# Optimization experiments

Measured on AMD Instinct MI355X. Metric: run time of the kernel, lower is better.

## Reference

```python
import jax, jax.numpy as jnp
import numpy as np

N = 100000
E = 1000000
IN_F, HID, NCLS = 128, 128, 40
EPS = 1e-5


def _gconv(h, src, dst, W, b):
    # DGL GraphConv with norm='both', allow_zero_in_degree=True (degrees clamped to >=1).
    ones = jnp.ones(src.shape, jnp.float32)
    dout = jnp.clip(jax.ops.segment_sum(ones, src, num_segments=N), 1.0)   # out-degree of src nodes
    din = jnp.clip(jax.ops.segment_sum(ones, dst, num_segments=N), 1.0)    # in-degree of dst nodes
    x = (h * jax.lax.rsqrt(dout)[:, None]) @ W            # [N, out] matmul-first (linear commutes with sum-aggregation)
    y = jax.ops.segment_sum(x[src], dst, num_segments=N)  # SpMM: scatter-add over edges
    y = y * jax.lax.rsqrt(din)[:, None]
    return y + b if b is not None else y


def _bn(h, gamma, beta):
    # BatchNorm1d training-mode math over the node dimension (biased variance).
    m = jnp.mean(h, axis=0)
    v = jnp.mean(jnp.square(h - m), axis=0)
    return (h - m) * jax.lax.rsqrt(v + EPS) * gamma + beta


def setup_inputs() -> dict:
    key = jax.random.key(0)
    ks = jax.random.split(key, 16)
    feat = jax.random.normal(ks[0], (N, IN_F), jnp.float32)
    src0 = jax.random.randint(ks[1], (E,), 0, N, jnp.int32)
    dst0 = jax.random.randint(ks[2], (E,), 0, N, jnp.int32)
    src1 = jax.random.randint(ks[3], (E,), 0, N, jnp.int32)
    dst1 = jax.random.randint(ks[4], (E,), 0, N, jnp.int32)
    order_attn = jax.random.uniform(ks[5], (2,), jnp.float32)
    s = lambda d_in, d_out: 1.0 / np.sqrt(d_in)
    W0 = jax.random.uniform(ks[6], (IN_F, HID), jnp.float32, -s(IN_F, HID), s(IN_F, HID))
    W1 = jax.random.uniform(ks[7], (HID, HID), jnp.float32, -s(HID, HID), s(HID, HID))
    W2 = jax.random.uniform(ks[8], (HID, NCLS), jnp.float32, -s(HID, NCLS), s(HID, NCLS))
    b2 = jnp.zeros((NCLS,), jnp.float32)
    L0 = jax.random.uniform(ks[9], (IN_F, HID), jnp.float32, -s(IN_F, HID), s(IN_F, HID))
    L1 = jax.random.uniform(ks[10], (HID, HID), jnp.float32, -s(HID, HID), s(HID, HID))
    L2 = jax.random.uniform(ks[11], (HID, NCLS), jnp.float32, -s(HID, NCLS), s(HID, NCLS))
    gamma0 = jnp.ones((HID,), jnp.float32); beta0 = jnp.zeros((HID,), jnp.float32)
    gamma1 = jnp.ones((HID,), jnp.float32); beta1 = jnp.zeros((HID,), jnp.float32)
    return dict(feat=feat, src0=src0, dst0=dst0, src1=src1, dst1=dst1, order_attn=order_attn,
                W0=W0, W1=W1, W2=W2, b2=b2, L0=L0, L1=L1, L2=L2,
                gamma0=gamma0, beta0=beta0, gamma1=gamma1, beta1=beta1)


def reference(feat, src0, dst0, src1, dst1, order_attn, W0, W1, W2, b2, L0, L1, L2,
              gamma0, beta0, gamma1, beta1):
    # Multi-graph path (len(graph)==2, n_layers==3, use_linear=True); dropout = identity (eval).
    h = feat
    # layer 0: order_attn-weighted combination of two adjacency variants
    conv1 = _gconv(h, src0, dst0, W0, None)
    conv2 = _gconv(h, src1, dst1, W0, None)
    conv = order_attn[0] * conv1 + order_attn[1] * conv2
    h = conv + h @ L0
    h = jax.nn.relu(_bn(h, gamma0, beta0))
    # layer 1 (convs[-2]) on graph[0]
    h = _gconv(h, src0, dst0, W1, None) + h @ L1
    h = jax.nn.relu(_bn(h, gamma1, beta1))
    # layer 2 (convs[-1]) on graph[0], with bias
    h = _gconv(h, src0, dst0, W2, b2) + h @ L2
    return h
```

## Files before the change

kernel.cpp:

```cpp
#include <hip/hip_runtime.h>
#include <math.h>

#define N_NODES 100000
#define N_EDGES 1000000
#define F 128
#define NC 40
#define BN_EPS 1e-5f
#define CH 32
#define EC (N_EDGES / CH)
#define WIN0 65536
#define NB1 (N_NODES - WIN0)
#define PROW (N_NODES / 4)

typedef unsigned int uint;
typedef unsigned short ushort;
typedef __attribute__((ext_vector_type(8))) short vbf8;
typedef __attribute__((ext_vector_type(4))) float vf4;

__device__ __forceinline__ float bf_lo(uint v) { return __uint_as_float(v << 16); }
__device__ __forceinline__ float bf_hi(uint v) { return __uint_as_float(v & 0xffff0000u); }
__device__ __forceinline__ ushort f2bf(float f) {
  uint u = __float_as_uint(f);
  u = u + 0x7fffu + ((u >> 16) & 1u);
  return (ushort)(u >> 16);
}
__device__ __forceinline__ uint pk2(float a, float b) {
  return (uint)f2bf(a) | ((uint)f2bf(b) << 16);
}

__global__ __launch_bounds__(256) void hist_count_k(
    const int* __restrict__ s0, const int* __restrict__ d0,
    const int* __restrict__ s1, const int* __restrict__ d1,
    unsigned* __restrict__ partial) {
  __shared__ unsigned bins[16384];
  int c = blockIdx.x, w = blockIdx.y, a = blockIdx.z;
  const int* keys = (a == 0) ? s0 : (a == 1) ? d0 : (a == 2) ? s1 : d1;
  int base = w * WIN0;
  int nb = w ? NB1 : WIN0;
  int nwords = nb >> 2;
  int t = threadIdx.x;
  for (int i = t; i < nwords; i += 256) bins[i] = 0;
  __syncthreads();
  int e0 = c * EC;
  for (int e = e0 + t; e < e0 + EC; e += 256) {
    int b = keys[e] - base;
    if ((unsigned)b < (unsigned)nb)
      atomicAdd(&bins[b >> 2], 1u << ((b & 3) * 8));
  }
  __syncthreads();
  unsigned* dst = partial + (size_t)(a * CH + c) * PROW + (w ? (WIN0 >> 2) : 0);
  for (int i = t; i < nwords; i += 256) dst[i] = bins[i];
}

__global__ __launch_bounds__(256) void deg_reduce_k(
    unsigned* __restrict__ partial, float* __restrict__ rs4, ushort* __restrict__ rsO01u,
    int* __restrict__ degIn0, int* __restrict__ degIn1,
    float* __restrict__ st0, float* __restrict__ st1) {
  int word = blockIdx.x * 256 + threadIdx.x;
  if (blockIdx.y == 0 && word < 256) { st0[word] = 0.f; st1[word] = 0.f; }
  if (word >= PROW) return;
  int a = blockIdx.y;
  bool din = (a == 1) || (a == 3);
  unsigned r0 = 0, r1 = 0, r2 = 0, r3 = 0;
  unsigned* rowp = partial + (size_t)a * CH * PROW + word;
  for (int c = 0; c < CH; ++c) {
    unsigned* p = rowp + (size_t)c * PROW;
    unsigned v = *p;
    if (din) *p = r0 | (r1 << 8) | (r2 << 16) | (r3 << 24);
    r0 += v & 255u; r1 += (v >> 8) & 255u; r2 += (v >> 16) & 255u; r3 += (v >> 24) & 255u;
  }
  int b = word * 4;
  float4 r;
  r.x = rsqrtf((float)max(r0, 1u));
  r.y = rsqrtf((float)max(r1, 1u));
  r.z = rsqrtf((float)max(r2, 1u));
  r.w = rsqrtf((float)max(r3, 1u));
  *(float4*)&rs4[(size_t)a * N_NODES + b] = r;
  if (a == 0) {
    rsO01u[2 * (b + 0)] = f2bf(r.x); rsO01u[2 * (b + 1)] = f2bf(r.y);
    rsO01u[2 * (b + 2)] = f2bf(r.z); rsO01u[2 * (b + 3)] = f2bf(r.w);
  }
  if (a == 2) {
    rsO01u[2 * (b + 0) + 1] = f2bf(r.x); rsO01u[2 * (b + 1) + 1] = f2bf(r.y);
    rsO01u[2 * (b + 2) + 1] = f2bf(r.z); rsO01u[2 * (b + 3) + 1] = f2bf(r.w);
  }
  if (a == 1) { degIn0[b] = r0; degIn0[b + 1] = r1; degIn0[b + 2] = r2; degIn0[b + 3] = r3; }
  if (a == 3) { degIn1[b] = r0; degIn1[b + 1] = r1; degIn1[b + 2] = r2; degIn1[b + 3] = r3; }
}

__global__ void scan_local_k(const int* __restrict__ cnt0, const int* __restrict__ cnt1,
                             int* __restrict__ out0, int* __restrict__ out1,
                             int* __restrict__ bsum) {
  __shared__ int lds[256];
  const int* cnt = blockIdx.y ? cnt1 : cnt0;
  int* out = blockIdx.y ? out1 : out0;
  int base = blockIdx.x * 2048;
  int t = threadIdx.x;
  int v[8];
  int s = 0;
#pragma unroll
  for (int j = 0; j < 8; ++j) {
    int idx = base + t * 8 + j;
    v[j] = (idx < N_NODES) ? cnt[idx] : 0;
    s += v[j];
  }
  lds[t] = s;
  __syncthreads();
  for (int off = 1; off < 256; off <<= 1) {
    int x = (t >= off) ? lds[t - off] : 0;
    __syncthreads();
    lds[t] += x;
    __syncthreads();
  }
  int excl = lds[t] - s;
  if (t == 255) bsum[blockIdx.y * 64 + blockIdx.x] = lds[255];
  int run = excl;
#pragma unroll
  for (int j = 0; j < 8; ++j) {
    int idx = base + t * 8 + j;
    if (idx < N_NODES) out[idx] = run;
    run += v[j];
  }
}

__global__ void scan_top_k(int* bsum, int nb) {
  int w = threadIdx.x >> 6, t = threadIdx.x & 63;
  int* b = bsum + w * 64;
  int orig = (t < nb) ? b[t] : 0;
  int v = orig;
  for (int off = 1; off < 64; off <<= 1) {
    int u = __shfl_up(v, off);
    if (t >= off) v += u;
  }
  if (t < nb) b[t] = v - orig;
}

__global__ void scan_apply_k(int* __restrict__ rp0, int* __restrict__ rp1,
                             const int* __restrict__ bsum) {
  int* rp = blockIdx.y ? rp1 : rp0;
  const int* bs = bsum + blockIdx.y * 64;
  int i = blockIdx.x * 256 + threadIdx.x;
  if (i < N_NODES) rp[i] += bs[i >> 11];
  if (i == 0) rp[N_NODES] = N_EDGES;
}

__global__ __launch_bounds__(256) void csr_fill2_k(
    const int* __restrict__ src0, const int* __restrict__ dst0, const int* __restrict__ rp0g,
    int* __restrict__ csr0g,
    const int* __restrict__ src1, const int* __restrict__ dst1, const int* __restrict__ rp1g,
    int* __restrict__ csr1g, const unsigned* __restrict__ partial) {
  __shared__ unsigned bins[16384];
  int c = blockIdx.x, w = blockIdx.y, g = blockIdx.z;
  const int* src = g ? src1 : src0;
  const int* dst = g ? dst1 : dst0;
  const int* rp = g ? rp1g : rp0g;
  int* csr = g ? csr1g : csr0g;
  int aIdx = g ? 3 : 1;
  int base = w * WIN0;
  int nb = w ? NB1 : WIN0;
  int nwords = nb >> 2;
  const unsigned* sp = partial + (size_t)(aIdx * CH + c) * PROW + (w ? (WIN0 >> 2) : 0);
  int t = threadIdx.x;
  for (int i = t; i < nwords; i += 256) bins[i] = sp[i];
  __syncthreads();
  int e0 = c * EC;
  for (int e = e0 + t; e < e0 + EC; e += 256) {
    int d = dst[e];
    int b = d - base;
    if ((unsigned)b < (unsigned)nb) {
      int sh = (b & 3) * 8;
      unsigned old = atomicAdd(&bins[b >> 2], 1u << sh);
      int off = (old >> sh) & 255;
      csr[rp[d] + off] = src[e];
    }
  }
}

__global__ __launch_bounds__(256) void pack_all_k(
    const float* __restrict__ x, uint* __restrict__ y,
    const float* __restrict__ Wa, const float* __restrict__ Wb,
    const float* __restrict__ Wc, const float* __restrict__ Wd,
    ushort* __restrict__ pk) {
  int b = blockIdx.x;
  int t = threadIdx.x;
  if (b < 1024) {
    size_t total = (size_t)N_NODES * F / 8;
    for (size_t idx = b * 256 + t; idx < total; idx += (size_t)1024 * 256) {
      float4 v1 = ((const float4*)x)[idx * 2];
      float4 v2 = ((const float4*)x)[idx * 2 + 1];
      uint4 o;
      o.x = pk2(v1.x, v1.y);
      o.y = pk2(v1.z, v1.w);
      o.z = pk2(v2.x, v2.y);
      o.w = pk2(v2.z, v2.w);
      ((uint4*)y)[idx] = o;
    }
  } else {
    int bb = b - 1024;
    int m = bb >> 3;
    int idx = (bb & 7) * 256 + t;
    const float* W = (m == 0) ? Wa : (m == 1) ? Wb : (m == 2) ? Wc : Wd;
    int lane = idx & 63;
    int nt = (idx >> 6) & 7;
    int ks = idx >> 9;
    int j = (lane & 15) + nt * 16;
    int kb = (lane >> 4) * 8 + ks * 32;
    ushort v[8];
#pragma unroll
    for (int q = 0; q < 8; ++q) v[q] = f2bf(W[(size_t)(kb + q) * F + j]);
    *(uint4*)(pk + (size_t)m * 16384 + (size_t)idx * 8) = *(uint4*)v;
  }
}

__global__ __launch_bounds__(256) void gather_dual_half_k(
    const uint* __restrict__ xbf, const float* __restrict__ attn,
    const uint* __restrict__ rsO01,
    const float* __restrict__ rsI0, const int* __restrict__ rp0, const int* __restrict__ csr0,
    const float* __restrict__ rsI1, const int* __restrict__ rp1, const int* __restrict__ csr1,
    uint* __restrict__ outbf) {
  int node = blockIdx.x * 4 + (threadIdx.x >> 6);
  int lane = threadIdx.x & 63;
  int half = lane >> 5, l = lane & 31;
  int b0 = rp0[node], n0 = rp0[node + 1] - b0;
  int b1 = rp1[node], n1 = rp1[node + 1] - b1;
  int T = n0 + n1;
  int h = (T + 1) >> 1;
  int e = half ? h : 0;
  int eend = half ? T : h;
  float w0 = attn[0] * rsI0[node];
  float w1 = attn[1] * rsI1[node];
  const int* p0 = csr0 + b0;
  const int* p1 = csr1 + b1 - n0;
  const uint2* xr = (const uint2*)xbf;
  float a0 = 0.f, a1 = 0.f, a2 = 0.f, a3 = 0.f;
  for (; e + 1 < eend; e += 2) {
    bool gA = e >= n0, gB = (e + 1) >= n0;
    int sA = (gA ? p1 : p0)[e];
    int sB = (gB ? p1 : p0)[e + 1];
    uint rA = rsO01[sA], rB = rsO01[sB];
    float cA = gA ? w1 * bf_hi(rA) : w0 * bf_lo(rA);
    float cB = gB ? w1 * bf_hi(rB) : w0 * bf_lo(rB);
    uint2 vA = xr[(size_t)sA * 32 + l];
    uint2 vB = xr[(size_t)sB * 32 + l];
    a0 = fmaf(bf_lo(vA.x), cA, a0); a1 = fmaf(bf_hi(vA.x), cA, a1);
    a2 = fmaf(bf_lo(vA.y), cA, a2); a3 = fmaf(bf_hi(vA.y), cA, a3);
    a0 = fmaf(bf_lo(vB.x), cB, a0); a1 = fmaf(bf_hi(vB.x), cB, a1);
    a2 = fmaf(bf_lo(vB.y), cB, a2); a3 = fmaf(bf_hi(vB.y), cB, a3);
  }
  if (e < eend) {
    bool gA = e >= n0;
    int sA = (gA ? p1 : p0)[e];
    uint rA = rsO01[sA];
    float cA = gA ? w1 * bf_hi(rA) : w0 * bf_lo(rA);
    uint2 vA = xr[(size_t)sA * 32 + l];
    a0 = fmaf(bf_lo(vA.x), cA, a0); a1 = fmaf(bf_hi(vA.x), cA, a1);
    a2 = fmaf(bf_lo(vA.y), cA, a2); a3 = fmaf(bf_hi(vA.y), cA, a3);
  }
  a0 += __shfl_xor(a0, 32);
  a1 += __shfl_xor(a1, 32);
  a2 += __shfl_xor(a2, 32);
  a3 += __shfl_xor(a3, 32);
  if (half == 0)
    ((uint2*)outbf)[(size_t)node * 32 + l] = make_uint2(pk2(a0, a1), pk2(a2, a3));
}

__global__ __launch_bounds__(256) void gather_half_k(
    const uint* __restrict__ xbf, const float* __restrict__ rsI,
    const int* __restrict__ rp, const int* __restrict__ csr,
    uint* __restrict__ outbf) {
  int node = blockIdx.x * 4 + (threadIdx.x >> 6);
  int lane = threadIdx.x & 63;
  int half = lane >> 5, l = lane & 31;
  int b0 = rp[node], T = rp[node + 1] - b0;
  int h = (T + 1) >> 1;
  int e = half ? h : 0;
  int eend = half ? T : h;
  const int* p = csr + b0;
  const uint2* xr = (const uint2*)xbf;
  float a0 = 0.f, a1 = 0.f, a2 = 0.f, a3 = 0.f;
  for (; e + 1 < eend; e += 2) {
    int sA = p[e], sB = p[e + 1];
    uint2 vA = xr[(size_t)sA * 32 + l];
    uint2 vB = xr[(size_t)sB * 32 + l];
    a0 += bf_lo(vA.x) + bf_lo(vB.x);
    a1 += bf_hi(vA.x) + bf_hi(vB.x);
    a2 += bf_lo(vA.y) + bf_lo(vB.y);
    a3 += bf_hi(vA.y) + bf_hi(vB.y);
  }
  if (e < eend) {
    int sA = p[e];
    uint2 vA = xr[(size_t)sA * 32 + l];
    a0 += bf_lo(vA.x); a1 += bf_hi(vA.x);
    a2 += bf_lo(vA.y); a3 += bf_hi(vA.y);
  }
  a0 += __shfl_xor(a0, 32);
  a1 += __shfl_xor(a1, 32);
  a2 += __shfl_xor(a2, 32);
  a3 += __shfl_xor(a3, 32);
  float sd = rsI[node];
  if (half == 0)
    ((uint2*)outbf)[(size_t)node * 32 + l] =
        make_uint2(pk2(a0 * sd, a1 * sd), pk2(a2 * sd, a3 * sd));
}

__global__ void gather40_add_k(const uint* __restrict__ x2bf, const float* __restrict__ rsI,
                               const int* __restrict__ rp, const int* __restrict__ csr,
                               float* __restrict__ out) {
  int node = (blockIdx.x * 256 + threadIdx.x) >> 5;
  int lane = threadIdx.x & 31;
  if (node >= N_NODES || lane >= 20) return;
  float l = 0.f, h = 0.f;
  int e = rp[node], end = rp[node + 1];
  for (; e + 3 < end; e += 4) {
    int sA = csr[e], sB = csr[e + 1], sC = csr[e + 2], sD = csr[e + 3];
    uint vA = x2bf[(size_t)sA * 20 + lane];
    uint vB = x2bf[(size_t)sB * 20 + lane];
    uint vC = x2bf[(size_t)sC * 20 + lane];
    uint vD = x2bf[(size_t)sD * 20 + lane];
    l += (bf_lo(vA) + bf_lo(vB)) + (bf_lo(vC) + bf_lo(vD));
    h += (bf_hi(vA) + bf_hi(vB)) + (bf_hi(vC) + bf_hi(vD));
  }
  for (; e < end; ++e) {
    uint vA = x2bf[(size_t)csr[e] * 20 + lane];
    l += bf_lo(vA);
    h += bf_hi(vA);
  }
  float sd = rsI[node];
  float2 p = *(float2*)(out + (size_t)node * NC + lane * 2);
  *(float2*)(out + (size_t)node * NC + lane * 2) = make_float2(p.x + l * sd, p.y + h * sd);
}

__global__ __launch_bounds__(256) void zscale_bf_k(
    const uint* __restrict__ h, const float* __restrict__ st,
    const float* __restrict__ gamma, const float* __restrict__ beta,
    const float* __restrict__ rs, uint* __restrict__ r0row, uint* __restrict__ zrow) {
  __shared__ float scl[128], shl[128];
  int t = threadIdx.x;
  if (t < 128) {
    float m = st[t] / (float)N_NODES;
    float v = st[128 + t] / (float)N_NODES - m * m;
    float s = gamma[t] * rsqrtf(fmaxf(v, 0.f) + BN_EPS);
    scl[t] = s;
    shl[t] = beta[t] - m * s;
  }
  __syncthreads();
  int idx = blockIdx.x * 256 + t;
  if (idx >= N_NODES * 16) return;
  int row = idx >> 4, kk = (idx & 15) * 8;
  uint4 v = ((const uint4*)h)[idx];
  float4 sc1 = *(float4*)&scl[kk];
  float4 sh1 = *(float4*)&shl[kk];
  float4 sc2 = *(float4*)&scl[kk + 4];
  float4 sh2 = *(float4*)&shl[kk + 4];
  float a0 = fmaxf(fmaf(bf_lo(v.x), sc1.x, sh1.x), 0.f);
  float a1 = fmaxf(fmaf(bf_hi(v.x), sc1.y, sh1.y), 0.f);
  float a2 = fmaxf(fmaf(bf_lo(v.y), sc1.z, sh1.z), 0.f);
  float a3 = fmaxf(fmaf(bf_hi(v.y), sc1.w, sh1.w), 0.f);
  float a4 = fmaxf(fmaf(bf_lo(v.z), sc2.x, sh2.x), 0.f);
  float a5 = fmaxf(fmaf(bf_hi(v.z), sc2.y, sh2.y), 0.f);
  float a6 = fmaxf(fmaf(bf_lo(v.w), sc2.z, sh2.z), 0.f);
  float a7 = fmaxf(fmaf(bf_hi(v.w), sc2.w, sh2.w), 0.f);
  uint4 o;
  o.x = pk2(a0, a1); o.y = pk2(a2, a3); o.z = pk2(a4, a5); o.w = pk2(a6, a7);
  ((uint4*)r0row)[idx] = o;
  float s = rs[row];
  uint4 z;
  z.x = pk2(a0 * s, a1 * s); z.y = pk2(a2 * s, a3 * s);
  z.z = pk2(a4 * s, a5 * s); z.w = pk2(a6 * s, a7 * s);
  ((uint4*)zrow)[idx] = z;
}

__global__ __launch_bounds__(256) void gemm_mfma_k(
    const ushort* __restrict__ A1, const ushort* __restrict__ A2,
    const ushort* __restrict__ pkA, const ushort* __restrict__ pkB,
    float* __restrict__ st, ushort* __restrict__ Cb) {
  __shared__ float sst[256];
  int t = threadIdx.x;
  int wave = t >> 6, lane = t & 63;
  int kgrp = lane >> 4, lrow = lane & 15;
  int arow = blockIdx.x * 64 + wave * 16 + lrow;
  bool rok = arow < N_NODES;
  const vbf8* a1p = (const vbf8*)(A1 + (size_t)(rok ? arow : 0) * F);
  const vbf8* a2p = (const vbf8*)(A2 + (size_t)(rok ? arow : 0) * F);
  const vbf8* wap = (const vbf8*)pkA + lane;
  const vbf8* wbp = (const vbf8*)pkB + lane;
  sst[t] = 0.f;
  __syncthreads();
  vbf8 zero = {0, 0, 0, 0, 0, 0, 0, 0};
  vf4 acc[8];
#pragma unroll
  for (int i = 0; i < 8; ++i) acc[i] = (vf4){0.f, 0.f, 0.f, 0.f};
#pragma unroll
  for (int ks = 0; ks < 4; ++ks) {
    vbf8 a1 = rok ? a1p[ks * 4 + kgrp] : zero;
    vbf8 a2 = rok ? a2p[ks * 4 + kgrp] : zero;
#pragma unroll
    for (int nt = 0; nt < 8; ++nt)
      acc[nt] = __builtin_amdgcn_mfma_f32_16x16x32_bf16(a1, wap[(ks * 8 + nt) * 64], acc[nt], 0, 0, 0);
#pragma unroll
    for (int nt = 0; nt < 8; ++nt)
      acc[nt] = __builtin_amdgcn_mfma_f32_16x16x32_bf16(a2, wbp[(ks * 8 + nt) * 64], acc[nt], 0, 0, 0);
  }
  int rbase = blockIdx.x * 64 + wave * 16 + kgrp * 4;
#pragma unroll
  for (int nt = 0; nt < 8; ++nt) {
    int col = nt * 16 + lrow;
#pragma unroll
    for (int r = 0; r < 4; ++r) {
      int row = rbase + r;
      if (row < N_NODES) Cb[(size_t)row * F + col] = f2bf(acc[nt][r]);
    }
  }
#pragma unroll
  for (int nt = 0; nt < 8; ++nt) {
    float s = acc[nt][0] + acc[nt][1] + acc[nt][2] + acc[nt][3];
    float q = acc[nt][0] * acc[nt][0] + acc[nt][1] * acc[nt][1] +
              acc[nt][2] * acc[nt][2] + acc[nt][3] * acc[nt][3];
    s += __shfl_xor(s, 16); q += __shfl_xor(q, 16);
    s += __shfl_xor(s, 32); q += __shfl_xor(q, 32);
    if (lane < 16) {
      atomicAdd(&sst[nt * 16 + lane], s);
      atomicAdd(&sst[128 + nt * 16 + lane], q);
    }
  }
  __syncthreads();
  atomicAdd(&st[t], sst[t]);
}

__global__ __launch_bounds__(256) void gemm40_dual_k(
    const uint* __restrict__ h1b, const float* __restrict__ st,
    const float* __restrict__ gamma, const float* __restrict__ beta,
    const float* __restrict__ W2, const float* __restrict__ L2, const float* __restrict__ bias,
    const float* __restrict__ rsO, uint* __restrict__ x2bf, float* __restrict__ outp) {
  __shared__ float Alds[25 * 128];
  __shared__ float Wl[128 * NC];
  __shared__ float Ll[128 * NC];
  __shared__ float scl[128], shl[128];
  int t = threadIdx.x;
  int r0 = blockIdx.x * 25;
  if (t < 128) {
    float m = st[t] / (float)N_NODES;
    float v = st[128 + t] / (float)N_NODES - m * m;
    float s = gamma[t] * rsqrtf(fmaxf(v, 0.f) + BN_EPS);
    scl[t] = s;
    shl[t] = beta[t] - m * s;
  }
  __syncthreads();
#pragma unroll
  for (int p = 0; p < 4; ++p) {
    int flat = t * 4 + p * 1024;
    if (flat < 25 * 128) {
      int lrr = flat >> 7, k = flat & 127;
      int row = r0 + lrr;
      float4 v = make_float4(0.f, 0.f, 0.f, 0.f);
      if (row < N_NODES) {
        uint2 u = *(const uint2*)(h1b + (size_t)row * 64 + (k >> 1));
        v = make_float4(bf_lo(u.x), bf_hi(u.x), bf_lo(u.y), bf_hi(u.y));
      }
      float4 scv = *(float4*)&scl[k];
      float4 shv = *(float4*)&shl[k];
      v.x = fmaxf(fmaf(v.x, scv.x, shv.x), 0.f);
      v.y = fmaxf(fmaf(v.y, scv.y, shv.y), 0.f);
      v.z = fmaxf(fmaf(v.z, scv.z, shv.z), 0.f);
      v.w = fmaxf(fmaf(v.w, scv.w, shv.w), 0.f);
      *(float4*)&Alds[flat] = v;
    }
  }
#pragma unroll
  for (int p = 0; p < 5; ++p) {
    int flat = t * 4 + p * 1024;
    if (flat < 128 * NC) {
      *(float4*)&Wl[flat] = *(const float4*)(W2 + flat);
      *(float4*)&Ll[flat] = *(const float4*)(L2 + flat);
    }
  }
  __syncthreads();
  if (t < 250) {
    int lrr = t / 10, cg = t % 10;
    float w0 = 0.f, w1 = 0.f, w2 = 0.f, w3 = 0.f;
    float l0 = 0.f, l1 = 0.f, l2 = 0.f, l3 = 0.f;
#pragma unroll 8
    for (int k = 0; k < 128; ++k) {
      float a = Alds[lrr * 128 + k];
      float4 w = *(float4*)&Wl[k * NC + cg * 4];
      float4 l = *(float4*)&Ll[k * NC + cg * 4];
      w0 = fmaf(a, w.x, w0); w1 = fmaf(a, w.y, w1);
      w2 = fmaf(a, w.z, w2); w3 = fmaf(a, w.w, w3);
      l0 = fmaf(a, l.x, l0); l1 = fmaf(a, l.y, l1);
      l2 = fmaf(a, l.z, l2); l3 = fmaf(a, l.w, l3);
    }
    int row = r0 + lrr;
    if (row < N_NODES) {
      float s = rsO[row];
      uint2 xo = make_uint2(pk2(w0 * s, w1 * s), pk2(w2 * s, w3 * s));
      *(uint2*)(x2bf + (size_t)row * 20 + cg * 2) = xo;
      float4 bv = *(const float4*)(bias + cg * 4);
      float4 oo = make_float4(l0 + bv.x, l1 + bv.y, l2 + bv.z, l3 + bv.w);
      *(float4*)(outp + (size_t)row * NC + cg * 4) = oo;
    }
  }
}

extern "C" void kernel_launch(void* const* d_in, const int* in_sizes, int n_in,
                              void* d_out, int out_size, void* d_ws, size_t ws_size,
                              hipStream_t stream) {
  const float* feat = (const float*)d_in[0];
  const int* src0 = (const int*)d_in[1];
  const int* dst0 = (const int*)d_in[2];
  const int* src1 = (const int*)d_in[3];
  const int* dst1 = (const int*)d_in[4];
  const float* attn = (const float*)d_in[5];
  const float* W0 = (const float*)d_in[6];
  const float* W1 = (const float*)d_in[7];
  const float* W2 = (const float*)d_in[8];
  const float* b2 = (const float*)d_in[9];
  const float* L0 = (const float*)d_in[10];
  const float* L1 = (const float*)d_in[11];
  const float* L2 = (const float*)d_in[12];
  const float* gamma0 = (const float*)d_in[13];
  const float* beta0 = (const float*)d_in[14];
  const float* gamma1 = (const float*)d_in[15];
  const float* beta1 = (const float*)d_in[16];
  float* out = (float*)d_out;

  char* base = (char*)d_ws;
  size_t off = 0;
  auto alloc = [&](size_t bytes) -> void* {
    void* p = base + off;
    off += (bytes + 255) & ~(size_t)255;
    return p;
  };
  unsigned* partial = (unsigned*)alloc((size_t)4 * CH * PROW * 4);
  float* rs4 = (float*)alloc(4 * (size_t)N_NODES * 4);
  uint* rsO01 = (uint*)alloc((size_t)N_NODES * 4);
  int* degIn0 = (int*)alloc(N_NODES * 4);
  int* degIn1 = (int*)alloc(N_NODES * 4);
  int* rp0 = (int*)alloc((N_NODES + 1) * 4);
  int* rp1 = (int*)alloc((N_NODES + 1) * 4);
  int* bsum = (int*)alloc(128 * 4);
  int* csr0 = (int*)alloc((size_t)N_EDGES * 4);
  int* csr1 = (int*)alloc((size_t)N_EDGES * 4);
  float* st0 = (float*)alloc(256 * 4);
  float* st1 = (float*)alloc(256 * 4);
  ushort* wpk = (ushort*)alloc((size_t)4 * 16384 * 2);
  uint* featbf = (uint*)alloc((size_t)N_NODES * 64 * 4);
  uint* aggbf = (uint*)alloc((size_t)N_NODES * 64 * 4);
  uint* hrow = (uint*)alloc((size_t)N_NODES * 64 * 4);
  uint* g1buf = (uint*)alloc((size_t)N_NODES * 64 * 4);
  if (off > ws_size) return;

  uint* r0row = aggbf;
  uint* zrow = featbf;
  uint* x2bf = featbf;

  float* rs_out0 = rs4;
  float* rs_in0 = rs4 + N_NODES;
  float* rs_in1 = rs4 + 3 * N_NODES;

  hist_count_k<<<dim3(CH, 2, 4), 256, 0, stream>>>(src0, dst0, src1, dst1, partial);
  deg_reduce_k<<<dim3((PROW + 255) / 256, 4), 256, 0, stream>>>(
      partial, rs4, (ushort*)rsO01, degIn0, degIn1, st0, st1);
  const int SCB = (N_NODES + 2047) / 2048;
  scan_local_k<<<dim3(SCB, 2), 256, 0, stream>>>(degIn0, degIn1, rp0, rp1, bsum);
  scan_top_k<<<1, 128, 0, stream>>>(bsum, SCB);
  scan_apply_k<<<dim3((N_NODES + 255) / 256, 2), 256, 0, stream>>>(rp0, rp1, bsum);
  csr_fill2_k<<<dim3(CH, 2, 2), 256, 0, stream>>>(src0, dst0, rp0, csr0,
                                                  src1, dst1, rp1, csr1, partial);

  pack_all_k<<<1056, 256, 0, stream>>>(feat, featbf, W0, L0, W1, L1, wpk);

  const int GB = (N_NODES + 63) / 64;

  gather_dual_half_k<<<N_NODES / 4, 256, 0, stream>>>(featbf, attn, rsO01, rs_in0, rp0, csr0,
                                                      rs_in1, rp1, csr1, aggbf);
  gemm_mfma_k<<<GB, 256, 0, stream>>>((ushort*)aggbf, (ushort*)featbf, wpk, wpk + 16384,
                                      st0, (ushort*)hrow);

  zscale_bf_k<<<N_NODES * 16 / 256, 256, 0, stream>>>(hrow, st0, gamma0, beta0, rs_out0,
                                                      r0row, zrow);
  gather_half_k<<<N_NODES / 4, 256, 0, stream>>>(zrow, rs_in0, rp0, csr0, g1buf);
  gemm_mfma_k<<<GB, 256, 0, stream>>>((ushort*)g1buf, (ushort*)r0row, wpk + 2 * 16384,
                                      wpk + 3 * 16384, st1, (ushort*)hrow);

  gemm40_dual_k<<<(N_NODES + 24) / 25, 256, 0, stream>>>(hrow, st1, gamma1, beta1, W2, L2, b2,
                                                         rs_out0, x2bf, out);
  gather40_add_k<<<(N_NODES * 32 + 255) / 256, 256, 0, stream>>>(x2bf, rs_in0, rp0, csr0, out);
}
```

Measured before the change: 520.5 us.

## Fuse BatchNorm+ReLU into layer-1 gather and GEMM, drop zscale pass

Removes the standalone zscale kernel that wrote normalized and degree-scaled bf16 copies of the hidden state. The layer-1 gather now applies BN scale/shift, ReLU and the source out-degree scale per gathered edge. A new GEMM variant applies BN+ReLU to its second operand while loading it. Gather loops in both gather kernels are also unrolled to four edges for more memory-level parallelism. This saves a full read and two full writes of the hidden matrix, in exchange for extra per-edge ALU work and an in-place hrow read/write in the GEMM that is safe only because each wave reads and writes its own rows.

```diff
diff --git a/kernel.cpp b/kernel.cpp
--- a/kernel.cpp
+++ b/kernel.cpp
@@ -224,16 +224,39 @@
   int b0 = rp0[node], n0 = rp0[node + 1] - b0;
   int b1 = rp1[node], n1 = rp1[node + 1] - b1;
   int T = n0 + n1;
-  int h = (T + 1) >> 1;
-  int e = half ? h : 0;
-  int eend = half ? T : h;
+  int mid = (T + 1) >> 1;
+  int e = half ? mid : 0;
+  int eend = half ? T : mid;
   float w0 = attn[0] * rsI0[node];
   float w1 = attn[1] * rsI1[node];
   const int* p0 = csr0 + b0;
   const int* p1 = csr1 + b1 - n0;
   const uint2* xr = (const uint2*)xbf;
   float a0 = 0.f, a1 = 0.f, a2 = 0.f, a3 = 0.f;
-  for (; e + 1 < eend; e += 2) {
+  for (; e + 3 < eend; e += 4) {
+    int s0 = (e >= n0 ? p1 : p0)[e];
+    int s1 = (e + 1 >= n0 ? p1 : p0)[e + 1];
+    int s2 = (e + 2 >= n0 ? p1 : p0)[e + 2];
+    int s3 = (e + 3 >= n0 ? p1 : p0)[e + 3];
+    uint r0v = rsO01[s0], r1v = rsO01[s1], r2v = rsO01[s2], r3v = rsO01[s3];
+    uint2 v0 = xr[(size_t)s0 * 32 + l];
+    uint2 v1 = xr[(size_t)s1 * 32 + l];
+    uint2 v2 = xr[(size_t)s2 * 32 + l];
+    uint2 v3 = xr[(size_t)s3 * 32 + l];
+    float c0 = (e >= n0) ? w1 * bf_hi(r0v) : w0 * bf_lo(r0v);
+    float c1 = (e + 1 >= n0) ? w1 * bf_hi(r1v) : w0 * bf_lo(r1v);
+    float c2 = (e + 2 >= n0) ? w1 * bf_hi(r2v) : w0 * bf_lo(r2v);
+    float c3 = (e + 3 >= n0) ? w1 * bf_hi(r3v) : w0 * bf_lo(r3v);
+    a0 = fmaf(bf_lo(v0.x), c0, a0); a1 = fmaf(bf_hi(v0.x), c0, a1);
+    a2 = fmaf(bf_lo(v0.y), c0, a2); a3 = fmaf(bf_hi(v0.y), c0, a3);
+    a0 = fmaf(bf_lo(v1.x), c1, a0); a1 = fmaf(bf_hi(v1.x), c1, a1);
+    a2 = fmaf(bf_lo(v1.y), c1, a2); a3 = fmaf(bf_hi(v1.y), c1, a3);
+    a0 = fmaf(bf_lo(v2.x), c2, a0); a1 = fmaf(bf_hi(v2.x), c2, a1);
+    a2 = fmaf(bf_lo(v2.y), c2, a2); a3 = fmaf(bf_hi(v2.y), c2, a3);
+    a0 = fmaf(bf_lo(v3.x), c3, a0); a1 = fmaf(bf_hi(v3.x), c3, a1);
+    a2 = fmaf(bf_lo(v3.y), c3, a2); a3 = fmaf(bf_hi(v3.y), c3, a3);
+  }
+  if (e + 1 < eend) {
     bool gA = e >= n0, gB = (e + 1) >= n0;
     int sA = (gA ? p1 : p0)[e];
     int sB = (gB ? p1 : p0)[e + 1];
@@ -246,6 +269,7 @@
     a2 = fmaf(bf_lo(vA.y), cA, a2); a3 = fmaf(bf_hi(vA.y), cA, a3);
     a0 = fmaf(bf_lo(vB.x), cB, a0); a1 = fmaf(bf_hi(vB.x), cB, a1);
     a2 = fmaf(bf_lo(vB.y), cB, a2); a3 = fmaf(bf_hi(vB.y), cB, a3);
+    e += 2;
   }
   if (e < eend) {
     bool gA = e >= n0;
@@ -264,34 +288,64 @@
     ((uint2*)outbf)[(size_t)node * 32 + l] = make_uint2(pk2(a0, a1), pk2(a2, a3));
 }
 
-__global__ __launch_bounds__(256) void gather_half_k(
-    const uint* __restrict__ xbf, const float* __restrict__ rsI,
-    const int* __restrict__ rp, const int* __restrict__ csr,
+__global__ __launch_bounds__(256) void gather_half_bn_k(
+    const uint* __restrict__ xbf, const float* __restrict__ st,
+    const float* __restrict__ gamma, const float* __restrict__ beta,
+    const float* __restrict__ rsO,
+    const float* __restrict__ rsI, const int* __restrict__ rp, const int* __restrict__ csr,
     uint* __restrict__ outbf) {
   int node = blockIdx.x * 4 + (threadIdx.x >> 6);
   int lane = threadIdx.x & 63;
   int half = lane >> 5, l = lane & 31;
+  float sc[4], sh[4];
+#pragma unroll
+  for (int j = 0; j < 4; ++j) {
+    int c = 4 * l + j;
+    float m = st[c] * (1.f / (float)N_NODES);
+    float v = st[128 + c] * (1.f / (float)N_NODES) - m * m;
+    float s = gamma[c] * rsqrtf(fmaxf(v, 0.f) + BN_EPS);
+    sc[j] = s;
+    sh[j] = beta[c] - m * s;
+  }
   int b0 = rp[node], T = rp[node + 1] - b0;
-  int h = (T + 1) >> 1;
-  int e = half ? h : 0;
-  int eend = half ? T : h;
+  int mid = (T + 1) >> 1;
+  int e = half ? mid : 0;
+  int eend = half ? T : mid;
   const int* p = csr + b0;
   const uint2* xr = (const uint2*)xbf;
   float a0 = 0.f, a1 = 0.f, a2 = 0.f, a3 = 0.f;
-  for (; e + 1 < eend; e += 2) {
-    int sA = p[e], sB = p[e + 1];
+  for (; e + 3 < eend; e += 4) {
+    int s0 = p[e], s1 = p[e + 1], s2 = p[e + 2], s3 = p[e + 3];
+    float c0 = rsO[s0], c1 = rsO[s1], c2 = rsO[s2], c3 = rsO[s3];
+    uint2 v0 = xr[(size_t)s0 * 32 + l];
+    uint2 v1 = xr[(size_t)s1 * 32 + l];
+    uint2 v2 = xr[(size_t)s2 * 32 + l];
+    uint2 v3 = xr[(size_t)s3 * 32 + l];
+    a0 = fmaf(fmaxf(fmaf(bf_lo(v0.x), sc[0], sh[0]), 0.f), c0, a0);
+    a1 = fmaf(fmaxf(fmaf(bf_hi(v0.x), sc[1], sh[1]), 0.f), c0, a1);
+    a2 = fmaf(fmaxf(fmaf(bf_lo(v0.y), sc[2], sh[2]), 0.f), c0, a2);
+    a3 = fmaf(fmaxf(fmaf(bf_hi(v0.y), sc[3], sh[3]), 0.f), c0, a3);
+    a0 = fmaf(fmaxf(fmaf(bf_lo(v1.x), sc[0], sh[0]), 0.f), c1, a0);
+    a1 = fmaf(fmaxf(fmaf(bf_hi(v1.x), sc[1], sh[1]), 0.f), c1, a1);
+    a2 = fmaf(fmaxf(fmaf(bf_lo(v1.y), sc[2], sh[2]), 0.f), c1, a2);
+    a3 = fmaf(fmaxf(fmaf(bf_hi(v1.y), sc[3], sh[3]), 0.f), c1, a3);
+    a0 = fmaf(fmaxf(fmaf(bf_lo(v2.x), sc[0], sh[0]), 0.f), c2, a0);
+    a1 = fmaf(fmaxf(fmaf(bf_hi(v2.x), sc[1], sh[1]), 0.f), c2, a1);
+    a2 = fmaf(fmaxf(fmaf(bf_lo(v2.y), sc[2], sh[2]), 0.f), c2, a2);
+    a3 = fmaf(fmaxf(fmaf(bf_hi(v2.y), sc[3], sh[3]), 0.f), c2, a3);
+    a0 = fmaf(fmaxf(fmaf(bf_lo(v3.x), sc[0], sh[0]), 0.f), c3, a0);
+    a1 = fmaf(fmaxf(fmaf(bf_hi(v3.x), sc[1], sh[1]), 0.f), c3, a1);
+    a2 = fmaf(fmaxf(fmaf(bf_lo(v3.y), sc[2], sh[2]), 0.f), c3, a2);
+    a3 = fmaf(fmaxf(fmaf(bf_hi(v3.y), sc[3], sh[3]), 0.f), c3, a3);
+  }
+  for (; e < eend; ++e) {
+    int sA = p[e];
+    float cA = rsO[sA];
     uint2 vA = xr[(size_t)sA * 32 + l];
-    uint2 vB = xr[(size_t)sB * 32 + l];
-    a0 += bf_lo(vA.x) + bf_lo(vB.x);
-    a1 += bf_hi(vA.x) + bf_hi(vB.x);
-    a2 += bf_lo(vA.y) + bf_lo(vB.y);
-    a3 += bf_hi(vA.y) + bf_hi(vB.y);
-  }
-  if (e < eend) {
-    int sA = p[e];
-    uint2 vA = xr[(size_t)sA * 32 + l];
-    a0 += bf_lo(vA.x); a1 += bf_hi(vA.x);
-    a2 += bf_lo(vA.y); a3 += bf_hi(vA.y);
+    a0 = fmaf(fmaxf(fmaf(bf_lo(vA.x), sc[0], sh[0]), 0.f), cA, a0);
+    a1 = fmaf(fmaxf(fmaf(bf_hi(vA.x), sc[1], sh[1]), 0.f), cA, a1);
+    a2 = fmaf(fmaxf(fmaf(bf_lo(vA.y), sc[2], sh[2]), 0.f), cA, a2);
+    a3 = fmaf(fmaxf(fmaf(bf_hi(vA.y), sc[3], sh[3]), 0.f), cA, a3);
   }
   a0 += __shfl_xor(a0, 32);
   a1 += __shfl_xor(a1, 32);
@@ -330,46 +384,6 @@
   *(float2*)(out + (size_t)node * NC + lane * 2) = make_float2(p.x + l * sd, p.y + h * sd);
 }
 
-__global__ __launch_bounds__(256) void zscale_bf_k(
-    const uint* __restrict__ h, const float* __restrict__ st,
-    const float* __restrict__ gamma, const float* __restrict__ beta,
-    const float* __restrict__ rs, uint* __restrict__ r0row, uint* __restrict__ zrow) {
-  __shared__ float scl[128], shl[128];
-  int t = threadIdx.x;
-  if (t < 128) {
-    float m = st[t] / (float)N_NODES;
-    float v = st[128 + t] / (float)N_NODES - m * m;
-    float s = gamma[t] * rsqrtf(fmaxf(v, 0.f) + BN_EPS);
-    scl[t] = s;
-    shl[t] = beta[t] - m * s;
-  }
-  __syncthreads();
-  int idx = blockIdx.x * 256 + t;
-  if (idx >= N_NODES * 16) return;
-  int row = idx >> 4, kk = (idx & 15) * 8;
-  uint4 v = ((const uint4*)h)[idx];
-  float4 sc1 = *(float4*)&scl[kk];
-  float4 sh1 = *(float4*)&shl[kk];
-  float4 sc2 = *(float4*)&scl[kk + 4];
-  float4 sh2 = *(float4*)&shl[kk + 4];
-  float a0 = fmaxf(fmaf(bf_lo(v.x), sc1.x, sh1.x), 0.f);
-  float a1 = fmaxf(fmaf(bf_hi(v.x), sc1.y, sh1.y), 0.f);
-  float a2 = fmaxf(fmaf(bf_lo(v.y), sc1.z, sh1.z), 0.f);
-  float a3 = fmaxf(fmaf(bf_hi(v.y), sc1.w, sh1.w), 0.f);
-  float a4 = fmaxf(fmaf(bf_lo(v.z), sc2.x, sh2.x), 0.f);
-  float a5 = fmaxf(fmaf(bf_hi(v.z), sc2.y, sh2.y), 0.f);
-  float a6 = fmaxf(fmaf(bf_lo(v.w), sc2.z, sh2.z), 0.f);
-  float a7 = fmaxf(fmaf(bf_hi(v.w), sc2.w, sh2.w), 0.f);
-  uint4 o;
-  o.x = pk2(a0, a1); o.y = pk2(a2, a3); o.z = pk2(a4, a5); o.w = pk2(a6, a7);
-  ((uint4*)r0row)[idx] = o;
-  float s = rs[row];
-  uint4 z;
-  z.x = pk2(a0 * s, a1 * s); z.y = pk2(a2 * s, a3 * s);
-  z.z = pk2(a4 * s, a5 * s); z.w = pk2(a6 * s, a7 * s);
-  ((uint4*)zrow)[idx] = z;
-}
-
 __global__ __launch_bounds__(256) void gemm_mfma_k(
     const ushort* __restrict__ A1, const ushort* __restrict__ A2,
     const ushort* __restrict__ pkA, const ushort* __restrict__ pkB,
@@ -394,6 +408,86 @@
   for (int ks = 0; ks < 4; ++ks) {
     vbf8 a1 = rok ? a1p[ks * 4 + kgrp] : zero;
     vbf8 a2 = rok ? a2p[ks * 4 + kgrp] : zero;
+#pragma unroll
+    for (int nt = 0; nt < 8; ++nt)
+      acc[nt] = __builtin_amdgcn_mfma_f32_16x16x32_bf16(a1, wap[(ks * 8 + nt) * 64], acc[nt], 0, 0, 0);
+#pragma unroll
+    for (int nt = 0; nt < 8; ++nt)
+      acc[nt] = __builtin_amdgcn_mfma_f32_16x16x32_bf16(a2, wbp[(ks * 8 + nt) * 64], acc[nt], 0, 0, 0);
+  }
+  int rbase = blockIdx.x * 64 + wave * 16 + kgrp * 4;
+#pragma unroll
+  for (int nt = 0; nt < 8; ++nt) {
+    int col = nt * 16 + lrow;
+#pragma unroll
+    for (int r = 0; r < 4; ++r) {
+      int row = rbase + r;
+      if (row < N_NODES) Cb[(size_t)row * F + col] = f2bf(acc[nt][r]);
+    }
+  }
+#pragma unroll
+  for (int nt = 0; nt < 8; ++nt) {
+    float s = acc[nt][0] + acc[nt][1] + acc[nt][2] + acc[nt][3];
+    float q = acc[nt][0] * acc[nt][0] + acc[nt][1] * acc[nt][1] +
+              acc[nt][2] * acc[nt][2] + acc[nt][3] * acc[nt][3];
+    s += __shfl_xor(s, 16); q += __shfl_xor(q, 16);
+    s += __shfl_xor(s, 32); q += __shfl_xor(q, 32);
+    if (lane < 16) {
+      atomicAdd(&sst[nt * 16 + lane], s);
+      atomicAdd(&sst[128 + nt * 16 + lane], q);
+    }
+  }
+  __syncthreads();
+  atomicAdd(&st[t], sst[t]);
+}
+
+__global__ __launch_bounds__(256) void gemm_mfma_bn_k(
+    const ushort* __restrict__ A1, const ushort* __restrict__ A2,
+    const float* __restrict__ stin, const float* __restrict__ gamma,
+    const float* __restrict__ beta,
+    const ushort* __restrict__ pkA, const ushort* __restrict__ pkB,
+    float* __restrict__ st, ushort* __restrict__ Cb) {
+  __shared__ float sst[256];
+  __shared__ float scl[128], shl[128];
+  int t = threadIdx.x;
+  int wave = t >> 6, lane = t & 63;
+  int kgrp = lane >> 4, lrow = lane & 15;
+  int arow = blockIdx.x * 64 + wave * 16 + lrow;
+  bool rok = arow < N_NODES;
+  if (t < 128) {
+    float m = stin[t] * (1.f / (float)N_NODES);
+    float v = stin[128 + t] * (1.f / (float)N_NODES) - m * m;
+    float s = gamma[t] * rsqrtf(fmaxf(v, 0.f) + BN_EPS);
+    scl[t] = s;
+    shl[t] = beta[t] - m * s;
+  }
+  const vbf8* a1p = (const vbf8*)(A1 + (size_t)(rok ? arow : 0) * F);
+  const vbf8* a2p = (const vbf8*)(A2 + (size_t)(rok ? arow : 0) * F);
+  const vbf8* wap = (const vbf8*)pkA + lane;
+  const vbf8* wbp = (const vbf8*)pkB + lane;
+  sst[t] = 0.f;
+  __syncthreads();
+  vbf8 zero = {0, 0, 0, 0, 0, 0, 0, 0};
+  vf4 acc[8];
+#pragma unroll
+  for (int i = 0; i < 8; ++i) acc[i] = (vf4){0.f, 0.f, 0.f, 0.f};
+#pragma unroll
+  for (int ks = 0; ks < 4; ++ks) {
+    vbf8 a1 = rok ? a1p[ks * 4 + kgrp] : zero;
+    vbf8 a2 = zero;
+    if (rok) {
+      vbf8 a2r = a2p[ks * 4 + kgrp];
+      const float* scp = &scl[ks * 32 + kgrp * 8];
+      const float* shp = &shl[ks * 32 + kgrp * 8];
+      ushort o[8];
+#pragma unroll
+      for (int q = 0; q < 8; ++q) {
+        float f = __uint_as_float(((uint)(ushort)a2r[q]) << 16);
+        f = fmaxf(fmaf(f, scp[q], shp[q]), 0.f);
+        o[q] = f2bf(f);
+      }
+      a2 = *(vbf8*)o;
+    }
 #pragma unroll
     for (int nt = 0; nt < 8; ++nt)
       acc[nt] = __builtin_amdgcn_mfma_f32_16x16x32_bf16(a1, wap[(ks * 8 + nt) * 64], acc[nt], 0, 0, 0);
@@ -549,8 +643,6 @@
   uint* g1buf = (uint*)alloc((size_t)N_NODES * 64 * 4);
   if (off > ws_size) return;
 
-  uint* r0row = aggbf;
-  uint* zrow = featbf;
   uint* x2bf = featbf;
 
   float* rs_out0 = rs4;
@@ -576,11 +668,10 @@
   gemm_mfma_k<<<GB, 256, 0, stream>>>((ushort*)aggbf, (ushort*)featbf, wpk, wpk + 16384,
                                       st0, (ushort*)hrow);
 
-  zscale_bf_k<<<N_NODES * 16 / 256, 256, 0, stream>>>(hrow, st0, gamma0, beta0, rs_out0,
-                                                      r0row, zrow);
-  gather_half_k<<<N_NODES / 4, 256, 0, stream>>>(zrow, rs_in0, rp0, csr0, g1buf);
-  gemm_mfma_k<<<GB, 256, 0, stream>>>((ushort*)g1buf, (ushort*)r0row, wpk + 2 * 16384,
-                                      wpk + 3 * 16384, st1, (ushort*)hrow);
+  gather_half_bn_k<<<N_NODES / 4, 256, 0, stream>>>(hrow, st0, gamma0, beta0, rs_out0,
+                                                    rs_in0, rp0, csr0, g1buf);
+  gemm_mfma_bn_k<<<GB, 256, 0, stream>>>((ushort*)g1buf, (ushort*)hrow, st0, gamma0, beta0,
+                                         wpk + 2 * 16384, wpk + 3 * 16384, st1, (ushort*)hrow);
 
   gemm40_dual_k<<<(N_NODES + 24) / 25, 256, 0, stream>>>(hrow, st1, gamma1, beta1, W2, L2, b2,
                                                          rs_out0, x2bf, out);
```

After: 502.7 us. -3.4%, faster.
